# Optimization experiments

Measured on AMD Instinct MI355X. Metric: run time of the kernel, lower is better.

Reference implementation:

```python
import jax, jax.numpy as jnp
import numpy as np

D_MODEL = 2048
N_HEADS = 16
HEAD_DIM = D_MODEL // N_HEADS
B, T = 2, 2048


def setup_inputs() -> dict:
    key = jax.random.key(0)
    ks = jax.random.split(key, 7)
    s = 0.02
    return {
        "x": jax.random.normal(ks[0], (B, T, D_MODEL), dtype=jnp.float32),
        "w_qkv": jax.random.normal(ks[1], (D_MODEL, 3 * D_MODEL), dtype=jnp.float32) * s,
        "w_proj": jax.random.normal(ks[2], (D_MODEL, D_MODEL), dtype=jnp.float32) * s,
        "w_ff1": jax.random.normal(ks[3], (D_MODEL, 4 * D_MODEL), dtype=jnp.float32) * s,
        "b_ff1": jnp.zeros((4 * D_MODEL,), dtype=jnp.float32),
        "w_ff2": jax.random.normal(ks[4], (4 * D_MODEL, D_MODEL), dtype=jnp.float32) * s,
        "b_ff2": jnp.zeros((D_MODEL,), dtype=jnp.float32),
    }


def reference(x, w_qkv, w_proj, w_ff1, b_ff1, w_ff2, b_ff2):
    Bs, Ts, C = x.shape
    H, hd = N_HEADS, HEAD_DIM
    # fused qkv projection
    qkv = jnp.einsum("btc,cd->btd", x, w_qkv)
    q, k, v = jnp.split(qkv, 3, axis=-1)
    # (B, T, C) -> (B, H, T, hd)
    q = q.reshape(Bs, Ts, H, hd).transpose(0, 2, 1, 3)
    k = k.reshape(Bs, Ts, H, hd).transpose(0, 2, 1, 3)
    v = v.reshape(Bs, Ts, H, hd).transpose(0, 2, 1, 3)
    # paged KV write + gather round-trip (empty cache, n_kv_head == n_heads)
    # is the identity on k, v; attention is causal SDPA over the full cache.
    scale = 1.0 / jnp.sqrt(jnp.asarray(hd, dtype=x.dtype))
    scores = jnp.einsum("bhqd,bhkd->bhqk", q, k) * scale
    causal = jnp.tril(jnp.ones((Ts, Ts), dtype=bool))
    scores = jnp.where(causal, scores, jnp.finfo(scores.dtype).min)
    attn = jax.nn.softmax(scores, axis=-1)
    out = jnp.einsum("bhqk,bhkd->bhqd", attn, v)  # (B, H, T, hd)
    out = out.transpose(0, 2, 1, 3).reshape(Bs, Ts, C)
    attn_out = jnp.einsum("btc,cd->btd", out, w_proj)
    # feed-forward with exact GELU (torch nn.GELU default)
    h = jax.nn.gelu(jnp.einsum("btc,cf->btf", x, w_ff1) + b_ff1, approximate=False)
    ff_out = jnp.einsum("btf,fc->btc", h, w_ff2) + b_ff2
    return x + attn_out + ff_out
```

## Files before the change

kernel.cpp:

```cpp
#include <hip/hip_runtime.h>
#include <hip/hip_bf16.h>
#include <cmath>

typedef __bf16 bf16x8 __attribute__((ext_vector_type(8)));
typedef float f32x4 __attribute__((ext_vector_type(4)));
typedef unsigned short u16;
typedef unsigned int u32;

#define DEV __device__ __forceinline__

static constexpr int BB = 2;
static constexpr int T = 2048;
static constexpr int DM = 2048;
static constexpr int NH = 16;
static constexpr int HD = 128;
static constexpr int FF = 8192;
static constexpr int M = BB * T;
static constexpr int NQKV = 3 * DM;

DEV u16 f2b(float f) {
  u32 u = __builtin_bit_cast(u32, f);
  u = (u + 0x7FFFu + ((u >> 16) & 1u)) >> 16;
  return (u16)u;
}
DEV float b2f(u16 h) {
  u32 u = ((u32)h) << 16;
  return __builtin_bit_cast(float, u);
}

DEV void gload16(const u16* g, const u16* l) {
  __builtin_amdgcn_global_load_lds(
      (const __attribute__((address_space(1))) void*)(uintptr_t)g,
      (__attribute__((address_space(3))) void*)(unsigned)(uintptr_t)l,
      16, 0, 0);
}


__global__ void cvt_f32_to_bf16(const float* __restrict__ in, u16* __restrict__ out, int n4) {
  int i = blockIdx.x * blockDim.x + threadIdx.x;
  if (i >= n4) return;
  float4 v = reinterpret_cast<const float4*>(in)[i];
  ushort4 o;
  o.x = f2b(v.x); o.y = f2b(v.y); o.z = f2b(v.z); o.w = f2b(v.w);
  reinterpret_cast<ushort4*>(out)[i] = o;
}

__global__ void transpose_cvt(const float* __restrict__ W, u16* __restrict__ Wt, int K, int N) {
  __shared__ float tile[32][33];
  int nb = blockIdx.x * 32, kb = blockIdx.y * 32;
  int tx = threadIdx.x & 31, ty = threadIdx.x >> 5;
#pragma unroll
  for (int r = 0; r < 32; r += 8)
    tile[ty + r][tx] = W[(size_t)(kb + ty + r) * N + nb + tx];
  __syncthreads();
#pragma unroll
  for (int r = 0; r < 32; r += 8)
    Wt[(size_t)(nb + ty + r) * K + kb + tx] = f2b(tile[tx][ty + r]);
}

template <int EPI>
__global__ __launch_bounds__(512, 4) void gemm_bf16(
    const u16* __restrict__ A, const u16* __restrict__ Bt, int Ndim, int K, int gx,
    u16* __restrict__ out_bf, float* __restrict__ out_f32,
    const float* __restrict__ bias,
    const float* __restrict__ resid_f32, const u16* __restrict__ resid_bf) {
  __shared__ __align__(16) u16 lds[3 * (256 + 128) * 32];
  const int t = threadIdx.x;
  const int nwg = gridDim.x, cpx = nwg >> 3;
  const int wg = (blockIdx.x & 7) * cpx + (blockIdx.x >> 3);
  const int m0 = (wg / gx) * 256, n0 = (wg % gx) * 128;
  const int wave = t >> 6, lane = t & 63;
  const int wm = wave >> 1, wn = wave & 1;
  const int lr = lane & 15, lk = lane >> 4;

  u16* cA = lds;                   u16* cB = lds + 8192;
  u16* nA = lds + 12288;           u16* nB = lds + 12288 + 8192;
  u16* sA = lds + 2 * 12288;       u16* sB = lds + 2 * 12288 + 8192;

  const int sk = (((lane & 3) ^ ((lane >> 3) & 3))) * 8;
  const u16* gA0 = &A[(size_t)(m0 + wave * 16 + (lane >> 2)) * K + sk];
  const u16* gA1 = gA0 + (size_t)128 * K;
  const u16* gB0 = &Bt[(size_t)(n0 + wave * 16 + (lane >> 2)) * K + sk];

  const int wbase = wave * 512;

  auto stage = [&](u16* dA, u16* dB) {
    gload16(gA0, dA + wbase);
    gload16(gA1, dA + 4096 + wbase);
    gload16(gB0, dB + wbase);
    gA0 += 32; gA1 += 32; gB0 += 32;
  };

  const int NT = K >> 5;

  stage(cA, cB);
  stage(nA, nB);
  __builtin_amdgcn_sched_barrier(0);
  asm volatile("s_waitcnt vmcnt(3)" ::: "memory");
  __builtin_amdgcn_s_barrier();
  __builtin_amdgcn_sched_barrier(0);

  f32x4 acc[4][4] = {};

  const int rcol = (lk ^ ((lr >> 1) & 3)) * 8;

  for (int kt = 0; kt < NT; ++kt) {
    if (kt + 2 < NT) stage(sA, sB);
    bf16x8 af[4], bfr[4];
#pragma unroll
    for (int i = 0; i < 4; ++i) {
      af[i]  = *reinterpret_cast<const bf16x8*>(&cA[(wm * 64 + i * 16 + lr) * 32 + rcol]);
      bfr[i] = *reinterpret_cast<const bf16x8*>(&cB[(wn * 64 + i * 16 + lr) * 32 + rcol]);
    }
#pragma unroll
    for (int i = 0; i < 4; ++i)
#pragma unroll
      for (int j = 0; j < 4; ++j)
        acc[i][j] = __builtin_amdgcn_mfma_f32_16x16x32_bf16(af[i], bfr[j], acc[i][j], 0, 0, 0);
    if (kt + 1 < NT) {
      __builtin_amdgcn_sched_barrier(0);
      if (kt + 2 < NT) asm volatile("s_waitcnt vmcnt(3)" ::: "memory");
      else             asm volatile("s_waitcnt vmcnt(0)" ::: "memory");
      __builtin_amdgcn_s_barrier();
      __builtin_amdgcn_sched_barrier(0);
      u16* tA = cA; u16* tB = cB;
      cA = nA; cB = nB; nA = sA; nB = sB; sA = tA; sB = tB;
    }
  }

#pragma unroll
  for (int i = 0; i < 4; ++i) {
#pragma unroll
    for (int j = 0; j < 4; ++j) {
#pragma unroll
      for (int r = 0; r < 4; ++r) {
        int gr = m0 + wm * 64 + i * 16 + (lane >> 4) * 4 + r;
        int gc = n0 + wn * 64 + j * 16 + (lane & 15);
        float v = acc[i][j][r];
        if constexpr (EPI == 0) {
          int part = gc >> 11, cc = gc & 2047;
          int head = cc >> 7, d = cc & 127;
          int b = gr >> 11, tt = gr & 2047;
          out_bf[(size_t)part * M * DM + (((size_t)(b * NH + head) * T + tt) * HD + d)] = f2b(v);
        } else if constexpr (EPI == 1) {
          out_bf[(size_t)gr * Ndim + gc] = f2b(v);
        } else if constexpr (EPI == 2) {
          v += bias[gc];
          float u = v * (v * v * 0.044715f + 1.0f) * 0.7978845608028654f;
          float e = exp2f(u * 2.885390081777927f);
          float th = 1.0f - 2.0f / (e + 1.0f);
          v = 0.5f * v * (1.0f + th);
          out_bf[(size_t)gr * Ndim + gc] = f2b(v);
        } else if constexpr (EPI == 3) {
          v += bias[gc] + resid_f32[(size_t)gr * Ndim + gc] + b2f(resid_bf[(size_t)gr * Ndim + gc]);
          out_f32[(size_t)gr * Ndim + gc] = v;
        } else {
          int hh = gr >> 7, d = gr & 127;
          int b = gc >> 11, tt = gc & 2047;
          out_bf[((size_t)(b * NH + hh) * HD + d) * T + tt] = f2b(v);
        }
      }
    }
  }
}

__global__ __launch_bounds__(256) void attn_fwd(
    const u16* __restrict__ qg, const u16* __restrict__ kg,
    const u16* __restrict__ vt, u16* __restrict__ outg) {
  __shared__ __align__(16) u16 lK[64 * 128];
  __shared__ __align__(16) u16 lVt[128 * 64];
  __shared__ __align__(16) u16 lP[4][16 * 72];
  const int t = threadIdx.x;
  const int qi = gridDim.x - 1 - blockIdx.x;
  const int bh = blockIdx.y;
  const int wv = t >> 6, lane = t & 63;
  const int lc = lane & 15, lg = lane >> 4;
  const size_t base = (size_t)bh * T * HD;
  const size_t vbase = (size_t)bh * HD * T;
  const int q0 = qi * 64;

  bf16x8 qf[4];
#pragma unroll
  for (int kk = 0; kk < 4; ++kk)
    qf[kk] = *reinterpret_cast<const bf16x8*>(
        &qg[base + (size_t)(q0 + wv * 16 + lc) * HD + kk * 32 + lg * 8]);

  f32x4 oacc[8] = {};
  float mrow[4], lrow[4];
#pragma unroll
  for (int r = 0; r < 4; ++r) { mrow[r] = -INFINITY; lrow[r] = 0.f; }

  const float scaleL = 0.08838834764831845f * 1.4426950408889634f;
  const int ntiles = qi + 1;
  for (int kt = 0; kt < ntiles; ++kt) {
    __syncthreads();
#pragma unroll
    for (int h = 0; h < 4; ++h) {
      int row = h * 16 + wv * 4 + (lane >> 4);
      int sb = ((lane & 15) * 16) ^ ((row & 7) << 4);
      gload16(&kg[base + (size_t)(kt * 64 + row) * HD + (sb >> 1)],
              (const u16*)((const char*)lK + (h * 256 + wv * 64) * 16));
    }
#pragma unroll
    for (int h = 0; h < 4; ++h) {
      int row = h * 32 + wv * 8 + (lane >> 3);
      int sb = ((lane & 7) * 16) ^ ((row & 7) << 4);
      gload16(&vt[vbase + (size_t)row * T + kt * 64 + (sb >> 1)],
              (const u16*)((const char*)lVt + (h * 256 + wv * 64) * 16));
    }
    __syncthreads();

    f32x4 s[4] = {};
#pragma unroll
    for (int nf = 0; nf < 4; ++nf) {
      int krow = nf * 16 + lc;
#pragma unroll
      for (int kk = 0; kk < 4; ++kk) {
        int dbyte = kk * 64 + lg * 16;
        bf16x8 kf = *reinterpret_cast<const bf16x8*>(
            reinterpret_cast<const char*>(lK) + krow * 256 + (dbyte ^ ((krow & 7) << 4)));
        s[nf] = __builtin_amdgcn_mfma_f32_16x16x32_bf16(qf[kk], kf, s[nf], 0, 0, 0);
      }
    }

    float rmax[4];
#pragma unroll
    for (int r = 0; r < 4; ++r) rmax[r] = -INFINITY;
#pragma unroll
    for (int nf = 0; nf < 4; ++nf) {
      int col = kt * 64 + nf * 16 + lc;
#pragma unroll
      for (int r = 0; r < 4; ++r) {
        int row = q0 + wv * 16 + lg * 4 + r;
        float sv = s[nf][r] * scaleL;
        if (col > row) sv = -INFINITY;
        s[nf][r] = sv;
        rmax[r] = fmaxf(rmax[r], sv);
      }
    }
#pragma unroll
    for (int mk = 1; mk < 16; mk <<= 1)
#pragma unroll
      for (int r = 0; r < 4; ++r)
        rmax[r] = fmaxf(rmax[r], __shfl_xor(rmax[r], mk));

    int need = 0;
#pragma unroll
    for (int r = 0; r < 4; ++r) need |= (rmax[r] > mrow[r] + 11.5f) ? 1 : 0;
    if (__any(need)) {
      float corr[4];
#pragma unroll
      for (int r = 0; r < 4; ++r) {
        float mnew = fmaxf(mrow[r], rmax[r]);
        corr[r] = exp2f(mrow[r] - mnew);
        mrow[r] = mnew;
        lrow[r] *= corr[r];
      }
#pragma unroll
      for (int dc = 0; dc < 8; ++dc)
#pragma unroll
        for (int r = 0; r < 4; ++r) oacc[dc][r] *= corr[r];
    }

#pragma unroll
    for (int nf = 0; nf < 4; ++nf) {
#pragma unroll
      for (int r = 0; r < 4; ++r) {
        float p = exp2f(s[nf][r] - mrow[r]);
        lrow[r] += p;
        lP[wv][(lg * 4 + r) * 72 + nf * 16 + lc] = f2b(p);
      }
    }
    bf16x8 pa[2];
#pragma unroll
    for (int kk = 0; kk < 2; ++kk)
      pa[kk] = *reinterpret_cast<const bf16x8*>(&lP[wv][lc * 72 + kk * 32 + lg * 8]);
#pragma unroll
    for (int dc = 0; dc < 8; ++dc) {
#pragma unroll
      for (int kk = 0; kk < 2; ++kk) {
        int vrow = dc * 16 + lc;
        int off = (kk * 64 + lg * 16) ^ ((vrow & 7) << 4);
        bf16x8 vf = *reinterpret_cast<const bf16x8*>(
            reinterpret_cast<const char*>(lVt) + vrow * 128 + off);
        oacc[dc] = __builtin_amdgcn_mfma_f32_16x16x32_bf16(pa[kk], vf, oacc[dc], 0, 0, 0);
      }
    }
  }

#pragma unroll
  for (int mk = 1; mk < 16; mk <<= 1)
#pragma unroll
    for (int r = 0; r < 4; ++r) lrow[r] += __shfl_xor(lrow[r], mk);

  const int b = bh >> 4, hh = bh & 15;
#pragma unroll
  for (int dc = 0; dc < 8; ++dc)
#pragma unroll
    for (int r = 0; r < 4; ++r) {
      int tt = q0 + wv * 16 + lg * 4 + r;
      int d = dc * 16 + lc;
      float o = oacc[dc][r] / lrow[r];
      outg[(size_t)(b * T + tt) * DM + hh * HD + d] = f2b(o);
    }
}


extern "C" void kernel_launch(void* const* d_in, const int* in_sizes, int n_in,
                              void* d_out, int out_size, void* d_ws, size_t ws_size,
                              hipStream_t stream) {
  const float* x      = (const float*)d_in[0];
  const float* w_qkv  = (const float*)d_in[1];
  const float* w_proj = (const float*)d_in[2];
  const float* w_ff1  = (const float*)d_in[3];
  const float* b_ff1  = (const float*)d_in[4];
  const float* w_ff2  = (const float*)d_in[5];
  const float* b_ff2  = (const float*)d_in[6];
  float* out = (float*)d_out;

  u16* ws = (u16*)d_ws;
  size_t o = 0;
  u16* x_bf      = ws + o; o += (size_t)M * DM;
  u16* wqkv_t    = ws + o; o += (size_t)NQKV * DM;
  u16* wproj_t   = ws + o; o += (size_t)DM * DM;
  u16* wff1_t    = ws + o; o += (size_t)FF * DM;
  u16* wff2_t    = ws + o; o += (size_t)DM * FF;
  u16* attn_proj = ws + o; o += (size_t)M * DM;
  u16* qbuf      = ws + o;
  u16* kbuf      = qbuf + (size_t)M * DM;
  u16* vtbuf     = kbuf + (size_t)M * DM;
  u16* attn_out  = vtbuf + (size_t)M * DM;
  u16* hbuf      = qbuf;

  cvt_f32_to_bf16<<<(M * DM / 4 + 255) / 256, 256, 0, stream>>>(x, x_bf, M * DM / 4);
  transpose_cvt<<<dim3(NQKV / 32, DM / 32), 256, 0, stream>>>(w_qkv, wqkv_t, DM, NQKV);
  transpose_cvt<<<dim3(DM / 32, DM / 32), 256, 0, stream>>>(w_proj, wproj_t, DM, DM);
  transpose_cvt<<<dim3(FF / 32, DM / 32), 256, 0, stream>>>(w_ff1, wff1_t, DM, FF);
  transpose_cvt<<<dim3(DM / 32, FF / 32), 256, 0, stream>>>(w_ff2, wff2_t, FF, DM);

  gemm_bf16<0><<<512, 512, 0, stream>>>(
      x_bf, wqkv_t, 4096, DM, 32, qbuf, nullptr, nullptr, nullptr, nullptr);

  gemm_bf16<4><<<256, 512, 0, stream>>>(
      wqkv_t + (size_t)4096 * DM, x_bf, M, DM, 32, vtbuf, nullptr, nullptr, nullptr, nullptr);

  attn_fwd<<<dim3(T / 64, BB * NH), 256, 0, stream>>>(qbuf, kbuf, vtbuf, attn_out);

  gemm_bf16<1><<<256, 512, 0, stream>>>(
      attn_out, wproj_t, DM, DM, 16, attn_proj, nullptr, nullptr, nullptr, nullptr);

  gemm_bf16<2><<<1024, 512, 0, stream>>>(
      x_bf, wff1_t, FF, DM, 64, hbuf, nullptr, b_ff1, nullptr, nullptr);

  gemm_bf16<3><<<256, 512, 0, stream>>>(
      hbuf, wff2_t, DM, FF, 16, nullptr, out, b_ff2, x, attn_proj);
}
```

Before: 676.9 us.

## Enlarge per-wave GEMM tiles and template tile width per launch

The GEMM kernel is templated on the number of wave columns, so the block tile becomes 256x128 (4 waves) or 256x256 (8 waves). Each wave now computes a 128x64 sub-tile with 8x4 MFMA accumulators instead of 4x4. Grid sizes and gx are adjusted for each GEMM. The aim is more operand reuse from LDS per MFMA and fewer blocks. The cost is doubled accumulator registers, occupancy limited to 2 blocks, and larger LDS use for the 256-wide variant.

```diff
diff --git a/kernel.cpp b/kernel.cpp
--- a/kernel.cpp
+++ b/kernel.cpp
@@ -58,37 +58,51 @@
     Wt[(size_t)(nb + ty + r) * K + kb + tx] = f2b(tile[tx][ty + r]);
 }
 
-template <int EPI>
-__global__ __launch_bounds__(512, 4) void gemm_bf16(
+template <int EPI, int NWN>
+__global__ __launch_bounds__(NWN * 128, 2) void gemm_bf16(
     const u16* __restrict__ A, const u16* __restrict__ Bt, int Ndim, int K, int gx,
     u16* __restrict__ out_bf, float* __restrict__ out_f32,
     const float* __restrict__ bias,
     const float* __restrict__ resid_f32, const u16* __restrict__ resid_bf) {
-  __shared__ __align__(16) u16 lds[3 * (256 + 128) * 32];
+  constexpr int BN = NWN * 64;
+  constexpr int NW = NWN * 2;
+  constexpr int AG = 256 / (16 * NW);
+  constexpr int BG = BN / (16 * NW);
+  constexpr int L = AG + BG;
+  constexpr int BUF = (256 + BN) * 32;
+  __shared__ __align__(16) u16 lds[3 * BUF];
   const int t = threadIdx.x;
   const int nwg = gridDim.x, cpx = nwg >> 3;
   const int wg = (blockIdx.x & 7) * cpx + (blockIdx.x >> 3);
-  const int m0 = (wg / gx) * 256, n0 = (wg % gx) * 128;
+  const int m0 = (wg / gx) * 256, n0 = (wg % gx) * BN;
   const int wave = t >> 6, lane = t & 63;
-  const int wm = wave >> 1, wn = wave & 1;
+  const int wm = wave & 1, wn = wave >> 1;
   const int lr = lane & 15, lk = lane >> 4;
 
-  u16* cA = lds;                   u16* cB = lds + 8192;
-  u16* nA = lds + 12288;           u16* nB = lds + 12288 + 8192;
-  u16* sA = lds + 2 * 12288;       u16* sB = lds + 2 * 12288 + 8192;
-
-  const int sk = (((lane & 3) ^ ((lane >> 3) & 3))) * 8;
-  const u16* gA0 = &A[(size_t)(m0 + wave * 16 + (lane >> 2)) * K + sk];
-  const u16* gA1 = gA0 + (size_t)128 * K;
-  const u16* gB0 = &Bt[(size_t)(n0 + wave * 16 + (lane >> 2)) * K + sk];
-
-  const int wbase = wave * 512;
+  u16* cA = lds;             u16* cB = lds + 8192;
+  u16* nA = lds + BUF;       u16* nB = lds + BUF + 8192;
+  u16* sA = lds + 2 * BUF;   u16* sB = lds + 2 * BUF + 8192;
+
+  const int sk = ((lane & 3) ^ ((lane >> 3) & 3)) * 8;
+  const u16* gA[AG];
+  const u16* gB[BG];
+#pragma unroll
+  for (int g = 0; g < AG; ++g)
+    gA[g] = &A[(size_t)(m0 + wave * (16 * AG) + g * 16 + (lane >> 2)) * K + sk];
+#pragma unroll
+  for (int g = 0; g < BG; ++g)
+    gB[g] = &Bt[(size_t)(n0 + wave * (16 * BG) + g * 16 + (lane >> 2)) * K + sk];
 
   auto stage = [&](u16* dA, u16* dB) {
-    gload16(gA0, dA + wbase);
-    gload16(gA1, dA + 4096 + wbase);
-    gload16(gB0, dB + wbase);
-    gA0 += 32; gA1 += 32; gB0 += 32;
+#pragma unroll
+    for (int g = 0; g < AG; ++g) { gload16(gA[g], dA + wave * (AG * 512) + g * 512); gA[g] += 32; }
+#pragma unroll
+    for (int g = 0; g < BG; ++g) { gload16(gB[g], dB + wave * (BG * 512) + g * 512); gB[g] += 32; }
+  };
+
+  auto waitL = [&]() {
+    if constexpr (L == 4) asm volatile("s_waitcnt vmcnt(4)" ::: "memory");
+    else                  asm volatile("s_waitcnt vmcnt(6)" ::: "memory");
   };
 
   const int NT = K >> 5;
@@ -96,30 +110,31 @@
   stage(cA, cB);
   stage(nA, nB);
   __builtin_amdgcn_sched_barrier(0);
-  asm volatile("s_waitcnt vmcnt(3)" ::: "memory");
+  waitL();
   __builtin_amdgcn_s_barrier();
   __builtin_amdgcn_sched_barrier(0);
 
-  f32x4 acc[4][4] = {};
+  f32x4 acc[8][4] = {};
 
   const int rcol = (lk ^ ((lr >> 1) & 3)) * 8;
 
   for (int kt = 0; kt < NT; ++kt) {
     if (kt + 2 < NT) stage(sA, sB);
-    bf16x8 af[4], bfr[4];
-#pragma unroll
-    for (int i = 0; i < 4; ++i) {
-      af[i]  = *reinterpret_cast<const bf16x8*>(&cA[(wm * 64 + i * 16 + lr) * 32 + rcol]);
-      bfr[i] = *reinterpret_cast<const bf16x8*>(&cB[(wn * 64 + i * 16 + lr) * 32 + rcol]);
-    }
-#pragma unroll
-    for (int i = 0; i < 4; ++i)
+    bf16x8 af[8], bfr[4];
+#pragma unroll
+    for (int i = 0; i < 8; ++i)
+      af[i] = *reinterpret_cast<const bf16x8*>(&cA[(wm * 128 + i * 16 + lr) * 32 + rcol]);
+#pragma unroll
+    for (int j = 0; j < 4; ++j)
+      bfr[j] = *reinterpret_cast<const bf16x8*>(&cB[(wn * 64 + j * 16 + lr) * 32 + rcol]);
+#pragma unroll
+    for (int i = 0; i < 8; ++i)
 #pragma unroll
       for (int j = 0; j < 4; ++j)
         acc[i][j] = __builtin_amdgcn_mfma_f32_16x16x32_bf16(af[i], bfr[j], acc[i][j], 0, 0, 0);
     if (kt + 1 < NT) {
       __builtin_amdgcn_sched_barrier(0);
-      if (kt + 2 < NT) asm volatile("s_waitcnt vmcnt(3)" ::: "memory");
+      if (kt + 2 < NT) waitL();
       else             asm volatile("s_waitcnt vmcnt(0)" ::: "memory");
       __builtin_amdgcn_s_barrier();
       __builtin_amdgcn_sched_barrier(0);
@@ -129,12 +144,12 @@
   }
 
 #pragma unroll
-  for (int i = 0; i < 4; ++i) {
+  for (int i = 0; i < 8; ++i) {
 #pragma unroll
     for (int j = 0; j < 4; ++j) {
 #pragma unroll
       for (int r = 0; r < 4; ++r) {
-        int gr = m0 + wm * 64 + i * 16 + (lane >> 4) * 4 + r;
+        int gr = m0 + wm * 128 + i * 16 + (lane >> 4) * 4 + r;
         int gc = n0 + wn * 64 + j * 16 + (lane & 15);
         float v = acc[i][j][r];
         if constexpr (EPI == 0) {
@@ -338,20 +353,20 @@
   transpose_cvt<<<dim3(FF / 32, DM / 32), 256, 0, stream>>>(w_ff1, wff1_t, DM, FF);
   transpose_cvt<<<dim3(DM / 32, FF / 32), 256, 0, stream>>>(w_ff2, wff2_t, FF, DM);
 
-  gemm_bf16<0><<<512, 512, 0, stream>>>(
-      x_bf, wqkv_t, 4096, DM, 32, qbuf, nullptr, nullptr, nullptr, nullptr);
-
-  gemm_bf16<4><<<256, 512, 0, stream>>>(
+  gemm_bf16<0, 4><<<256, 512, 0, stream>>>(
+      x_bf, wqkv_t, 4096, DM, 16, qbuf, nullptr, nullptr, nullptr, nullptr);
+
+  gemm_bf16<4, 2><<<256, 256, 0, stream>>>(
       wqkv_t + (size_t)4096 * DM, x_bf, M, DM, 32, vtbuf, nullptr, nullptr, nullptr, nullptr);
 
   attn_fwd<<<dim3(T / 64, BB * NH), 256, 0, stream>>>(qbuf, kbuf, vtbuf, attn_out);
 
-  gemm_bf16<1><<<256, 512, 0, stream>>>(
+  gemm_bf16<1, 2><<<256, 256, 0, stream>>>(
       attn_out, wproj_t, DM, DM, 16, attn_proj, nullptr, nullptr, nullptr, nullptr);
 
-  gemm_bf16<2><<<1024, 512, 0, stream>>>(
-      x_bf, wff1_t, FF, DM, 64, hbuf, nullptr, b_ff1, nullptr, nullptr);
-
-  gemm_bf16<3><<<256, 512, 0, stream>>>(
+  gemm_bf16<2, 4><<<512, 512, 0, stream>>>(
+      x_bf, wff1_t, FF, DM, 32, hbuf, nullptr, b_ff1, nullptr, nullptr);
+
+  gemm_bf16<3, 2><<<256, 256, 0, stream>>>(
       hbuf, wff2_t, DM, FF, 16, nullptr, out, b_ff2, x, attn_proj);
 }
```

Measured after the change: 670.0 us. Within noise of the previous version (-1.0%).

## Add 256x256-tile eight-wave phased GEMM for QK projection and FF1

Applied to the files above, without the earlier changes.

Adds a new GEMM kernel, gemm8, and uses it for the Q/K projection and the FF1+GELU GEMM. Each block computes a 256x256 output tile with a K-step of 64, double-buffered in 128 KB of LDS. Each k-step is split into four MFMA phases; global loads for the next stages are interleaved between phases, separated by barriers and s_setprio. The goal is higher arithmetic intensity per LDS and global load, and better overlap of memory traffic with MFMA, at the cost of one block per CU and a larger per-thread register footprint.

```diff
diff --git a/kernel.cpp b/kernel.cpp
--- a/kernel.cpp
+++ b/kernel.cpp
@@ -56,6 +56,172 @@
 #pragma unroll
   for (int r = 0; r < 32; r += 8)
     Wt[(size_t)(nb + ty + r) * K + kb + tx] = f2b(tile[tx][ty + r]);
+}
+
+template <int EPI>
+__global__ __launch_bounds__(512, 2) void gemm8(
+    const u16* __restrict__ A, const u16* __restrict__ Bt, int Ndim, int K, int gx,
+    u16* __restrict__ out_bf, const float* __restrict__ bias) {
+  __shared__ __align__(16) u16 lds[2 * 32768];
+  const int t = threadIdx.x;
+  const int nwg = gridDim.x, cpx = nwg >> 3;
+  const int wg = (blockIdx.x & 7) * cpx + (blockIdx.x >> 3);
+  const int m0 = (wg / gx) * 256, n0 = (wg % gx) * 256;
+  const int wave = t >> 6, lane = t & 63;
+  const int wm = wave >> 2, wn = wave & 3;
+  const int lr = lane & 15, lk = lane >> 4;
+
+  const int srow = t >> 3;
+  const int sc8 = ((t & 7) ^ (srow & 7)) * 8;
+  const u16* gA = &A[(size_t)(m0 + srow) * K + sc8];
+  const u16* gB = &Bt[(size_t)(n0 + srow) * K + sc8];
+  const int wls = wave * 512;
+
+  u16* buf0 = lds;
+  u16* buf1 = lds + 32768;
+
+#define STAGE_A(buf, h, kt)                                                      \
+  {                                                                              \
+    gload16(gA + (size_t)((h) * 128) * K + (kt) * 64, (buf) + (h) * 8192 + wls); \
+    gload16(gA + (size_t)((h) * 128 + 64) * K + (kt) * 64,                       \
+            (buf) + (h) * 8192 + 4096 + wls);                                    \
+  }
+#define STAGE_B(buf, h, kt)                                                      \
+  {                                                                              \
+    gload16(gB + (size_t)((h) * 128) * K + (kt) * 64,                            \
+            (buf) + 16384 + (h) * 8192 + wls);                                   \
+    gload16(gB + (size_t)((h) * 128 + 64) * K + (kt) * 64,                       \
+            (buf) + 16384 + (h) * 8192 + 4096 + wls);                            \
+  }
+#define PH_PRE                          \
+  __builtin_amdgcn_sched_barrier(0);    \
+  __builtin_amdgcn_s_barrier();         \
+  __builtin_amdgcn_sched_barrier(0);    \
+  __builtin_amdgcn_s_setprio(1);
+#define PH_POST                         \
+  __builtin_amdgcn_s_setprio(0);        \
+  __builtin_amdgcn_sched_barrier(0);    \
+  __builtin_amdgcn_s_barrier();         \
+  __builtin_amdgcn_sched_barrier(0);
+
+  const int NT = K >> 6;
+
+  STAGE_A(buf0, 0, 0); STAGE_A(buf0, 1, 0);
+  STAGE_B(buf0, 0, 0); STAGE_B(buf0, 1, 0);
+  STAGE_A(buf1, 0, 1); STAGE_B(buf1, 0, 1);
+  __builtin_amdgcn_sched_barrier(0);
+  asm volatile("s_waitcnt vmcnt(4)" ::: "memory");
+  __builtin_amdgcn_s_barrier();
+  __builtin_amdgcn_sched_barrier(0);
+
+  f32x4 acc[8][4] = {};
+  const int aBase = (wm * 128 + lr) * 64;
+  const int bBase = 16384 + (wn * 64 + lr) * 64;
+  const int c0 = (lk ^ (lr & 7)) * 8;
+  const int c1 = ((4 + lk) ^ (lr & 7)) * 8;
+
+  u16* cur = buf0;
+  u16* alt = buf1;
+  bf16x8 af[4][2], bq0[2][2], bq1[2][2];
+
+  for (int kt = 0; kt < NT; ++kt) {
+#pragma unroll
+    for (int i = 0; i < 4; ++i) {
+      af[i][0] = *(const bf16x8*)&cur[aBase + i * 1024 + c0];
+      af[i][1] = *(const bf16x8*)&cur[aBase + i * 1024 + c1];
+    }
+#pragma unroll
+    for (int j = 0; j < 2; ++j) {
+      bq0[j][0] = *(const bf16x8*)&cur[bBase + j * 1024 + c0];
+      bq0[j][1] = *(const bf16x8*)&cur[bBase + j * 1024 + c1];
+    }
+    if (kt + 1 < NT) STAGE_A(alt, 1, kt + 1);
+    PH_PRE;
+#pragma unroll
+    for (int i = 0; i < 4; ++i)
+#pragma unroll
+      for (int j = 0; j < 2; ++j)
+#pragma unroll
+        for (int kk = 0; kk < 2; ++kk)
+          acc[i][j] = __builtin_amdgcn_mfma_f32_16x16x32_bf16(af[i][kk], bq0[j][kk], acc[i][j], 0, 0, 0);
+    PH_POST;
+#pragma unroll
+    for (int j = 0; j < 2; ++j) {
+      bq1[j][0] = *(const bf16x8*)&cur[bBase + (2 + j) * 1024 + c0];
+      bq1[j][1] = *(const bf16x8*)&cur[bBase + (2 + j) * 1024 + c1];
+    }
+    if (kt + 1 < NT) STAGE_B(alt, 1, kt + 1);
+    PH_PRE;
+#pragma unroll
+    for (int i = 0; i < 4; ++i)
+#pragma unroll
+      for (int j = 0; j < 2; ++j)
+#pragma unroll
+        for (int kk = 0; kk < 2; ++kk)
+          acc[i][2 + j] = __builtin_amdgcn_mfma_f32_16x16x32_bf16(af[i][kk], bq1[j][kk], acc[i][2 + j], 0, 0, 0);
+    PH_POST;
+#pragma unroll
+    for (int i = 0; i < 4; ++i) {
+      af[i][0] = *(const bf16x8*)&cur[aBase + (4 + i) * 1024 + c0];
+      af[i][1] = *(const bf16x8*)&cur[aBase + (4 + i) * 1024 + c1];
+    }
+    if (kt + 2 < NT) STAGE_A(cur, 0, kt + 2);
+    PH_PRE;
+#pragma unroll
+    for (int i = 0; i < 4; ++i)
+#pragma unroll
+      for (int j = 0; j < 2; ++j)
+#pragma unroll
+        for (int kk = 0; kk < 2; ++kk)
+          acc[4 + i][2 + j] = __builtin_amdgcn_mfma_f32_16x16x32_bf16(af[i][kk], bq1[j][kk], acc[4 + i][2 + j], 0, 0, 0);
+    PH_POST;
+    if (kt + 2 < NT) STAGE_B(cur, 0, kt + 2);
+    PH_PRE;
+#pragma unroll
+    for (int i = 0; i < 4; ++i)
+#pragma unroll
+      for (int j = 0; j < 2; ++j)
+#pragma unroll
+        for (int kk = 0; kk < 2; ++kk)
+          acc[4 + i][j] = __builtin_amdgcn_mfma_f32_16x16x32_bf16(af[i][kk], bq0[j][kk], acc[4 + i][j], 0, 0, 0);
+    __builtin_amdgcn_s_setprio(0);
+    __builtin_amdgcn_sched_barrier(0);
+    if (kt + 2 < NT)      asm volatile("s_waitcnt vmcnt(4)" ::: "memory");
+    else if (kt + 1 < NT) asm volatile("s_waitcnt vmcnt(0)" ::: "memory");
+    __builtin_amdgcn_s_barrier();
+    __builtin_amdgcn_sched_barrier(0);
+    u16* tmp = cur; cur = alt; alt = tmp;
+  }
+#undef STAGE_A
+#undef STAGE_B
+#undef PH_PRE
+#undef PH_POST
+
+#pragma unroll
+  for (int i = 0; i < 8; ++i) {
+#pragma unroll
+    for (int j = 0; j < 4; ++j) {
+#pragma unroll
+      for (int r = 0; r < 4; ++r) {
+        int gr = m0 + wm * 128 + i * 16 + (lane >> 4) * 4 + r;
+        int gc = n0 + wn * 64 + j * 16 + (lane & 15);
+        float v = acc[i][j][r];
+        if constexpr (EPI == 0) {
+          int part = gc >> 11, cc = gc & 2047;
+          int head = cc >> 7, d = cc & 127;
+          int b = gr >> 11, tt = gr & 2047;
+          out_bf[(size_t)part * M * DM + (((size_t)(b * NH + head) * T + tt) * HD + d)] = f2b(v);
+        } else {
+          v += bias[gc];
+          float u = v * (v * v * 0.044715f + 1.0f) * 0.7978845608028654f;
+          float e = exp2f(u * 2.885390081777927f);
+          float th = 1.0f - 2.0f / (e + 1.0f);
+          v = 0.5f * v * (1.0f + th);
+          out_bf[(size_t)gr * Ndim + gc] = f2b(v);
+        }
+      }
+    }
+  }
 }
 
 template <int EPI>
@@ -77,7 +243,7 @@
   u16* nA = lds + 12288;           u16* nB = lds + 12288 + 8192;
   u16* sA = lds + 2 * 12288;       u16* sB = lds + 2 * 12288 + 8192;
 
-  const int sk = (((lane & 3) ^ ((lane >> 3) & 3))) * 8;
+  const int sk = ((lane & 3) ^ ((lane >> 3) & 3)) * 8;
   const u16* gA0 = &A[(size_t)(m0 + wave * 16 + (lane >> 2)) * K + sk];
   const u16* gA1 = gA0 + (size_t)128 * K;
   const u16* gB0 = &Bt[(size_t)(n0 + wave * 16 + (lane >> 2)) * K + sk];
@@ -101,7 +267,6 @@
   __builtin_amdgcn_sched_barrier(0);
 
   f32x4 acc[4][4] = {};
-
   const int rcol = (lk ^ ((lr >> 1) & 3)) * 8;
 
   for (int kt = 0; kt < NT; ++kt) {
@@ -137,19 +302,7 @@
         int gr = m0 + wm * 64 + i * 16 + (lane >> 4) * 4 + r;
         int gc = n0 + wn * 64 + j * 16 + (lane & 15);
         float v = acc[i][j][r];
-        if constexpr (EPI == 0) {
-          int part = gc >> 11, cc = gc & 2047;
-          int head = cc >> 7, d = cc & 127;
-          int b = gr >> 11, tt = gr & 2047;
-          out_bf[(size_t)part * M * DM + (((size_t)(b * NH + head) * T + tt) * HD + d)] = f2b(v);
-        } else if constexpr (EPI == 1) {
-          out_bf[(size_t)gr * Ndim + gc] = f2b(v);
-        } else if constexpr (EPI == 2) {
-          v += bias[gc];
-          float u = v * (v * v * 0.044715f + 1.0f) * 0.7978845608028654f;
-          float e = exp2f(u * 2.885390081777927f);
-          float th = 1.0f - 2.0f / (e + 1.0f);
-          v = 0.5f * v * (1.0f + th);
+        if constexpr (EPI == 1) {
           out_bf[(size_t)gr * Ndim + gc] = f2b(v);
         } else if constexpr (EPI == 3) {
           v += bias[gc] + resid_f32[(size_t)gr * Ndim + gc] + b2f(resid_bf[(size_t)gr * Ndim + gc]);
@@ -338,8 +491,7 @@
   transpose_cvt<<<dim3(FF / 32, DM / 32), 256, 0, stream>>>(w_ff1, wff1_t, DM, FF);
   transpose_cvt<<<dim3(DM / 32, FF / 32), 256, 0, stream>>>(w_ff2, wff2_t, FF, DM);
 
-  gemm_bf16<0><<<512, 512, 0, stream>>>(
-      x_bf, wqkv_t, 4096, DM, 32, qbuf, nullptr, nullptr, nullptr, nullptr);
+  gemm8<0><<<256, 512, 0, stream>>>(x_bf, wqkv_t, 4096, DM, 16, qbuf, nullptr);
 
   gemm_bf16<4><<<256, 512, 0, stream>>>(
       wqkv_t + (size_t)4096 * DM, x_bf, M, DM, 32, vtbuf, nullptr, nullptr, nullptr, nullptr);
@@ -349,8 +501,7 @@
   gemm_bf16<1><<<256, 512, 0, stream>>>(
       attn_out, wproj_t, DM, DM, 16, attn_proj, nullptr, nullptr, nullptr, nullptr);
 
-  gemm_bf16<2><<<1024, 512, 0, stream>>>(
-      x_bf, wff1_t, FF, DM, 64, hbuf, nullptr, b_ff1, nullptr, nullptr);
+  gemm8<2><<<512, 512, 0, stream>>>(x_bf, wff1_t, FF, DM, 32, hbuf, b_ff1);
 
   gemm_bf16<3><<<256, 512, 0, stream>>>(
       hbuf, wff2_t, DM, FF, 16, nullptr, out, b_ff2, x, attn_proj);
```

After: 655.8 us. 1.03x faster.
